# Kernel tuning notes

Hardware: AMD Instinct MI355X
Metric: run time of the kernel (lower is better)

The kernel has to match this reference:

```python
import jax, jax.numpy as jnp
import numpy as np

B, S, D, H = 4, 2048, 1024, 16
HD = D // H          # head_dim = 64
R = D // 2           # svd rank = int(D * svd_r), svd_r = 0.5


def setup_inputs() -> dict:
    key = jax.random.key(0)
    ks = jax.random.split(key, 12)
    sc = 0.02  # gpt2-style init scale
    return {
        "hidden_states": jax.random.normal(ks[0], (B, S, D), jnp.float32),
        # full Q projection (nn.Linear: weight [out, in])
        "WQ_w": jax.random.normal(ks[1], (D, D), jnp.float32) * sc,
        "WQ_b": jnp.zeros((D,), jnp.float32),
        # low-rank K projection: WK_A (no bias) then WK_B (bias)
        "WK_A_w": jax.random.normal(ks[2], (R, D), jnp.float32) * sc,
        "WK_B_w": jax.random.normal(ks[3], (D, R), jnp.float32) * sc,
        "WK_B_b": jnp.zeros((D,), jnp.float32),
        # low-rank V projection
        "WV_A_w": jax.random.normal(ks[4], (R, D), jnp.float32) * sc,
        "WV_B_w": jax.random.normal(ks[5], (D, R), jnp.float32) * sc,
        "WV_B_b": jnp.zeros((D,), jnp.float32),
        # output projection (HF Conv1D: weight [in, out], out = x @ W + b)
        "c_proj_w": jax.random.normal(ks[6], (D, D), jnp.float32) * sc,
        "c_proj_b": jnp.zeros((D,), jnp.float32),
    }


def reference(hidden_states, WQ_w, WQ_b, WK_A_w, WK_B_w, WK_B_b,
              WV_A_w, WV_B_w, WV_B_b, c_proj_w, c_proj_b):
    # projections (Q full-rank; K/V via SVD low-rank factors)
    q = hidden_states @ WQ_w.T + WQ_b                                  # [B,S,D]
    k = (hidden_states @ WK_A_w.T) @ WK_B_w.T + WK_B_b                 # [B,S,D]
    v = (hidden_states @ WV_A_w.T) @ WV_B_w.T + WV_B_b                 # [B,S,D]

    def split_heads(x):  # [B,S,D] -> [B,H,S,HD]
        return x.reshape(B, S, H, HD).transpose(0, 2, 1, 3)

    q, k, v = split_heads(q), split_heads(k), split_heads(v)

    # eager causal attention: QK^T / sqrt(head_dim), mask, softmax, PV
    scores = jnp.einsum('bhqd,bhkd->bhqk', q, k) / jnp.asarray(
        np.sqrt(HD), dtype=q.dtype)                                    # [B,H,S,S]
    causal = jnp.tril(jnp.ones((S, S), dtype=bool))
    scores = jnp.where(causal, scores, jnp.finfo(scores.dtype).min)
    attn = jax.nn.softmax(scores, axis=-1)                             # [B,H,S,S]
    # attn_dropout is identity (p=0 / eval mode)

    out = jnp.einsum('bhqk,bhkd->bqhd', attn, v).reshape(B, S, D)      # merge heads
    out = out @ c_proj_w + c_proj_b                                    # Conv1D c_proj
    # resid_dropout is identity (p=0 / eval mode)
    return out
```

## Files before the change

### kernel.cpp

```cpp
#include <hip/hip_runtime.h>

#define Bz 4
#define Sz 2048
#define Dz 1024
#define Hz 16
#define HDz 64
#define Rz 512
#define Mz (Bz * Sz)

typedef unsigned short u16;
typedef __bf16 bf16x8 __attribute__((ext_vector_type(8)));
typedef __bf16 bf16x4 __attribute__((ext_vector_type(4)));
typedef float f32x4 __attribute__((ext_vector_type(4)));
typedef u16 u16x8 __attribute__((ext_vector_type(8)));
typedef u16 u16x4 __attribute__((ext_vector_type(4)));

__device__ __forceinline__ u16 f2bf(float f) {
  unsigned u = __builtin_bit_cast(unsigned, f);
  u += 0x7fffu + ((u >> 16) & 1u);
  return (u16)(u >> 16);
}

#define GLDS(g, l)                                                              \
  __builtin_amdgcn_global_load_lds(                                             \
      (const __attribute__((address_space(1))) void*)(g),                       \
      (__attribute__((address_space(3))) void*)(l), 16, 0, 0)

__global__ void convert_bf16(const float* __restrict__ in, u16* __restrict__ out, int n) {
  int i = (blockIdx.x * blockDim.x + threadIdx.x) * 8;
  if (i >= n) return;
  float4 a = *(const float4*)(in + i);
  float4 b = *(const float4*)(in + i + 4);
  u16x8 r;
  r[0] = f2bf(a.x); r[1] = f2bf(a.y); r[2] = f2bf(a.z); r[3] = f2bf(a.w);
  r[4] = f2bf(b.x); r[5] = f2bf(b.y); r[6] = f2bf(b.z); r[7] = f2bf(b.w);
  *(u16x8*)(out + i) = r;
}

__global__ void transpose_convert(const float* __restrict__ in, u16* __restrict__ out,
                                  int R, int C) {
  __shared__ float t[32][33];
  int bx = blockIdx.x * 32, by = blockIdx.y * 32;
  int x = threadIdx.x, y = threadIdx.y;
#pragma unroll
  for (int j = 0; j < 32; j += 8) t[y + j][x] = in[(size_t)(by + y + j) * C + bx + x];
  __syncthreads();
#pragma unroll
  for (int j = 0; j < 32; j += 8)
    out[(size_t)(bx + y + j) * R + by + x] = f2bf(t[x][y + j]);
}

__global__ void make_biascat(const float* __restrict__ qb_, float* __restrict__ out) {
  int i = blockIdx.x * 256 + threadIdx.x;
  out[i] = (i < Dz) ? qb_[i] : 0.0f;
}

template <int MODE>
__global__ __launch_bounds__(256) void gemm_nt(const u16* __restrict__ A,
                                               const u16* __restrict__ W,
                                               const float* __restrict__ bias,
                                               void* __restrict__ Cv,
                                               int M, int N, int K, int lda) {
  __shared__ u16 As[128 * 32];
  __shared__ u16 Bs[128 * 32];
  const int tid = threadIdx.x;
  const int wid = tid >> 6, lane = tid & 63;
  const int nwg = gridDim.x * gridDim.y;
  const int id = blockIdx.y * gridDim.x + blockIdx.x;
  const int swz = (id & 7) * (nwg >> 3) + (id >> 3);
  const int bx = swz % gridDim.x, by = swz / gridDim.x;
  const int row0 = by * 128, col0 = bx * 128;
  const int wm = (wid >> 1) * 64, wn = (wid & 1) * 64;
  f32x4 acc[4][4] = {};
  const int srow = lane >> 2, scol = (lane & 3) * 8;
  const int frow = lane & 15, fk = (lane >> 4) * 8;

  for (int k0 = 0; k0 < K; k0 += 32) {
    __syncthreads();
#pragma unroll
    for (int it = 0; it < 2; ++it) {
      int c = it * 4 + wid;
      const u16* ga = A + (size_t)(row0 + c * 16 + srow) * lda + k0 + scol;
      const u16* gb = W + (size_t)(col0 + c * 16 + srow) * K + k0 + scol;
      GLDS(ga, As + c * 512);
      GLDS(gb, Bs + c * 512);
    }
    __syncthreads();
    bf16x8 af[4], bfr[4];
#pragma unroll
    for (int m = 0; m < 4; ++m) af[m] = *(const bf16x8*)(As + (wm + m * 16 + frow) * 32 + fk);
#pragma unroll
    for (int n = 0; n < 4; ++n) bfr[n] = *(const bf16x8*)(Bs + (wn + n * 16 + frow) * 32 + fk);
#pragma unroll
    for (int m = 0; m < 4; ++m)
#pragma unroll
      for (int n = 0; n < 4; ++n)
        acc[m][n] = __builtin_amdgcn_mfma_f32_16x16x32_bf16(af[m], bfr[n], acc[m][n], 0, 0, 0);
  }

  const int r4 = (lane >> 4) * 4, cc = lane & 15;
#pragma unroll
  for (int m = 0; m < 4; ++m)
#pragma unroll
    for (int n = 0; n < 4; ++n) {
      int col = col0 + wn + n * 16 + cc;
      float bv = bias[col];
      if constexpr (MODE == 2) {
        int rowb = row0 + wm + m * 16 + r4;
        size_t obase = (size_t)((rowb >> 11) * Hz + (col >> 6)) * ((size_t)HDz * Sz) +
                       (size_t)(col & 63) * Sz + (rowb & 2047);
        u16x4 w4;
#pragma unroll
        for (int j = 0; j < 4; ++j) w4[j] = f2bf(acc[m][n][j] + bv);
        *(u16x4*)((u16*)Cv + obase) = w4;
      } else {
#pragma unroll
        for (int j = 0; j < 4; ++j) {
          int row = row0 + wm + m * 16 + r4 + j;
          float v = acc[m][n][j] + bv;
          if constexpr (MODE == 0)
            ((u16*)Cv)[(size_t)row * N + col] = f2bf(v);
          else
            ((float*)Cv)[(size_t)row * N + col] = v;
        }
      }
    }
}

__device__ __forceinline__ void* lsw(void* base, int row, int bo) {
  return (char*)base + (((row << 7) + bo) ^ ((row & 7) << 4));
}

template <bool MASK>
__device__ __forceinline__ void tile_step(u16* Ks, u16* Vts, u16* Pw,
                                          int frow, int fhi, int qlocb, int koff,
                                          const bf16x8 (&qf)[2][2],
                                          f32x4 (&o)[4][2], float* rs) {
#pragma unroll
  for (int qs = 0; qs < 2; ++qs) {
    f32x4 s[4] = {};
#pragma unroll
    for (int dc = 0; dc < 2; ++dc)
#pragma unroll
      for (int c = 0; c < 4; ++c) {
        bf16x8 kf = *(const bf16x8*)lsw(Ks, c * 16 + frow, dc * 64 + fhi * 16);
        s[c] = __builtin_amdgcn_mfma_f32_16x16x32_bf16(kf, qf[qs][dc], s[c], 0, 0, 0);
      }
    const int qloc = qlocb + qs * 16 + frow;
#pragma unroll
    for (int c = 0; c < 4; ++c) {
      bf16x4 w;
#pragma unroll
      for (int j = 0; j < 4; ++j) {
        float v = __builtin_exp2f(s[c][j] * 0.18033688f);
        if (MASK) v = ((koff + c * 16 + fhi * 4 + j) <= qloc) ? v : 0.0f;
        rs[qs] += v;
        w[j] = (__bf16)v;
      }
      *(bf16x4*)lsw(Pw, qs * 16 + frow, c * 32 + fhi * 8) = w;
    }
  }
#pragma unroll
  for (int kc = 0; kc < 2; ++kc) {
    bf16x8 pa0 = *(const bf16x8*)lsw(Pw, frow, kc * 64 + fhi * 16);
    bf16x8 pa1 = *(const bf16x8*)lsw(Pw, 16 + frow, kc * 64 + fhi * 16);
#pragma unroll
    for (int n = 0; n < 4; ++n) {
      bf16x8 vf = *(const bf16x8*)lsw(Vts, n * 16 + frow, kc * 64 + fhi * 16);
      o[n][0] = __builtin_amdgcn_mfma_f32_16x16x32_bf16(vf, pa0, o[n][0], 0, 0, 0);
      o[n][1] = __builtin_amdgcn_mfma_f32_16x16x32_bf16(vf, pa1, o[n][1], 0, 0, 0);
    }
  }
}

__global__ __launch_bounds__(256, 2) void attn_kernel(const u16* __restrict__ Q,
                                                      const u16* __restrict__ Kg,
                                                      const u16* __restrict__ Vt,
                                                      u16* __restrict__ Og) {
  __shared__ __align__(16) u16 Ks[64 * 64];
  __shared__ __align__(16) u16 Vts[64 * 64];
  __shared__ __align__(16) u16 Ps[4][32 * 64];
  const int pr = blockIdx.x;
  const int qA = pr, qB = 15 - pr;
  const int bh = blockIdx.y;
  const int tid = threadIdx.x, wid = tid >> 6, lane = tid & 63;
  const size_t kbase = (size_t)(bh >> 4) * Sz * Dz + (size_t)(bh & 15) * HDz;
  const size_t qbase = (size_t)(bh >> 4) * Sz * 2048 + (size_t)(bh & 15) * HDz;
  const size_t vtb = (size_t)bh * HDz * Sz;
  const int frow = lane & 15, fhi = lane >> 4;
  const int q0A = qA * 128 + wid * 32, q0B = qB * 128 + wid * 32;

  bf16x8 qfA[2][2], qfB[2][2];
#pragma unroll
  for (int qs = 0; qs < 2; ++qs)
#pragma unroll
    for (int dc = 0; dc < 2; ++dc) {
      qfA[qs][dc] = *(const bf16x8*)(Q + qbase + (size_t)(q0A + qs * 16 + frow) * 2048 +
                                     dc * 32 + fhi * 8);
      qfB[qs][dc] = *(const bf16x8*)(Q + qbase + (size_t)(q0B + qs * 16 + frow) * 2048 +
                                     dc * 32 + fhi * 8);
    }

  f32x4 oA[4][2] = {}, oB[4][2] = {};
  float rsA[2] = {0.0f, 0.0f}, rsB[2] = {0.0f, 0.0f};

  const int r = tid >> 2, cb = (tid & 3) * 32;
  const u16* kgp = Kg + kbase + (size_t)r * Dz + (tid & 3) * 16;
  const u16* vgp = Vt + vtb + (size_t)r * Sz + (tid & 3) * 16;

  const int ntB = 2 * qB + 2;
  u16x8 ka = *(const u16x8*)(kgp);
  u16x8 kb2 = *(const u16x8*)(kgp + 8);
  u16x8 va = *(const u16x8*)(vgp);
  u16x8 vb2 = *(const u16x8*)(vgp + 8);

  for (int t = 0; t < ntB; ++t) {
    __syncthreads();
    *(u16x8*)lsw(Ks, r, cb) = ka;
    *(u16x8*)lsw(Ks, r, cb + 16) = kb2;
    *(u16x8*)lsw(Vts, r, cb) = va;
    *(u16x8*)lsw(Vts, r, cb + 16) = vb2;
    if (t + 1 < ntB) {
      const size_t ko = (size_t)(t + 1) * 64 * Dz;
      const size_t vo = (size_t)(t + 1) * 64;
      ka = *(const u16x8*)(kgp + ko);
      kb2 = *(const u16x8*)(kgp + ko + 8);
      va = *(const u16x8*)(vgp + vo);
      vb2 = *(const u16x8*)(vgp + vo + 8);
    }
    __syncthreads();

    if (64 * t <= q0B + 31) {
      if (t >= 2 * qB)
        tile_step<true>(Ks, Vts, Ps[wid], frow, fhi, wid * 32, (t - 2 * qB) * 64,
                        qfB, oB, rsB);
      else
        tile_step<false>(Ks, Vts, Ps[wid], frow, fhi, wid * 32, 0, qfB, oB, rsB);
    }
    if (64 * t <= q0A + 31) {
      if (t >= 2 * qA)
        tile_step<true>(Ks, Vts, Ps[wid], frow, fhi, wid * 32, (t - 2 * qA) * 64,
                        qfA, oA, rsA);
      else
        tile_step<false>(Ks, Vts, Ps[wid], frow, fhi, wid * 32, 0, qfA, oA, rsA);
    }
  }

#pragma unroll
  for (int x = 0; x < 2; ++x) {
    f32x4(&o)[4][2] = x ? oA : oB;
    float* rs = x ? rsA : rsB;
    const int q0 = x ? q0A : q0B;
#pragma unroll
    for (int qs = 0; qs < 2; ++qs) {
      float l = rs[qs];
      l += __shfl_xor(l, 16);
      l += __shfl_xor(l, 32);
      float inv = 1.0f / l;
      const size_t ob = kbase + (size_t)(q0 + qs * 16 + frow) * Dz;
#pragma unroll
      for (int n = 0; n < 4; ++n) {
        bf16x4 w;
#pragma unroll
        for (int j = 0; j < 4; ++j) w[j] = (__bf16)(o[n][qs][j] * inv);
        *(bf16x4*)(Og + ob + n * 16 + fhi * 4) = w;
      }
    }
  }
}

extern "C" void kernel_launch(void* const* d_in, const int* in_sizes, int n_in,
                              void* d_out, int out_size, void* d_ws, size_t ws_size,
                              hipStream_t stream) {
  const float* hs    = (const float*)d_in[0];
  const float* WQ_w  = (const float*)d_in[1];
  const float* WQ_b  = (const float*)d_in[2];
  const float* WKA_w = (const float*)d_in[3];
  const float* WKB_w = (const float*)d_in[4];
  const float* WKB_b = (const float*)d_in[5];
  const float* WVA_w = (const float*)d_in[6];
  const float* WVB_w = (const float*)d_in[7];
  const float* WVB_b = (const float*)d_in[8];
  const float* WC_w  = (const float*)d_in[9];
  const float* WC_b  = (const float*)d_in[10];
  float* out = (float*)d_out;

  char* p = (char*)d_ws;
  auto alloc = [&](size_t bytes) {
    char* r = p;
    p += (bytes + 255) & ~(size_t)255;
    return r;
  };
  u16* hsb   = (u16*)alloc((size_t)Mz * Dz * 2);
  u16* wcat  = (u16*)alloc((size_t)2048 * Dz * 2);
  u16* wkbb  = (u16*)alloc((size_t)Dz * Rz * 2);
  u16* wvbb  = (u16*)alloc((size_t)Dz * Rz * 2);
  u16* wcb   = (u16*)alloc((size_t)Dz * Dz * 2);
  float* bcat = (float*)alloc((size_t)2048 * 4);
  u16* QA    = (u16*)alloc((size_t)Mz * 2048 * 2);
  u16* Kb    = (u16*)alloc((size_t)Mz * Dz * 2);
  u16* Vtg   = (u16*)alloc((size_t)Mz * Dz * 2);
  u16* AOb   = hsb;

  convert_bf16<<<(Mz * Dz) / 8 / 256, 256, 0, stream>>>(hs, hsb, Mz * Dz);
  convert_bf16<<<(Dz * Dz) / 8 / 256, 256, 0, stream>>>(WQ_w, wcat, Dz * Dz);
  convert_bf16<<<(Rz * Dz) / 8 / 256, 256, 0, stream>>>(WKA_w, wcat + (size_t)Dz * Dz, Rz * Dz);
  convert_bf16<<<(Rz * Dz) / 8 / 256, 256, 0, stream>>>(WVA_w, wcat + (size_t)1536 * Dz, Rz * Dz);
  convert_bf16<<<(Dz * Rz) / 8 / 256, 256, 0, stream>>>(WKB_w, wkbb, Dz * Rz);
  convert_bf16<<<(Dz * Rz) / 8 / 256, 256, 0, stream>>>(WVB_w, wvbb, Dz * Rz);
  transpose_convert<<<dim3(Dz / 32, Dz / 32), dim3(32, 8), 0, stream>>>(WC_w, wcb, Dz, Dz);
  make_biascat<<<8, 256, 0, stream>>>(WQ_b, bcat);

  gemm_nt<0><<<dim3(2048 / 128, Mz / 128), 256, 0, stream>>>(hsb, wcat, bcat, QA,
                                                             Mz, 2048, Dz, Dz);
  gemm_nt<0><<<dim3(Dz / 128, Mz / 128), 256, 0, stream>>>(QA + Dz, wkbb, WKB_b, Kb,
                                                           Mz, Dz, Rz, 2048);
  gemm_nt<2><<<dim3(Dz / 128, Mz / 128), 256, 0, stream>>>(QA + 1536, wvbb, WVB_b, Vtg,
                                                           Mz, Dz, Rz, 2048);

  attn_kernel<<<dim3(Sz / 256, Bz * Hz), 256, 0, stream>>>(QA, Kb, Vtg, AOb);

  gemm_nt<1><<<dim3(Dz / 128, Mz / 128), 256, 0, stream>>>(AOb, wcb, WC_b, out,
                                                           Mz, Dz, Dz, Dz);
}
```

Measured before the change: 311.3 us.

## Add 256x256 tiled GEMM kernel and batch K/V up-projections into one launch

Adds a new GEMM kernel with 256x256 output tiles, 512 threads, 64-wide K steps, double-buffered LDS fed by global_load_lds, an XOR-swizzled LDS layout, workgroup id swizzling and raised MFMA priority. The QKV-A projection now uses it, and the K and V up-projections run together in one launch, selected by blockIdx.z. The old gemm_nt keeps only the fp32 output mode for c_proj. The aim is more data reuse per tile and fewer launches. The cost is much more LDS per block and more registers per thread, which could reduce occupancy.

Result: faster. 282.0 us (-9.4%).

```diff
diff --git a/kernel.cpp b/kernel.cpp
--- a/kernel.cpp
+++ b/kernel.cpp
@@ -105,8 +105,107 @@
     for (int n = 0; n < 4; ++n) {
       int col = col0 + wn + n * 16 + cc;
       float bv = bias[col];
-      if constexpr (MODE == 2) {
-        int rowb = row0 + wm + m * 16 + r4;
+#pragma unroll
+      for (int j = 0; j < 4; ++j) {
+        int row = row0 + wm + m * 16 + r4 + j;
+        ((float*)Cv)[(size_t)row * N + col] = acc[m][n][j] + bv;
+      }
+    }
+}
+
+__global__ __launch_bounds__(512, 2) void gemm256(
+    const u16* __restrict__ A0, const u16* __restrict__ W0,
+    const float* __restrict__ bias0, void* __restrict__ C0, int mode0,
+    const u16* __restrict__ A1, const u16* __restrict__ W1,
+    const float* __restrict__ bias1, void* __restrict__ C1, int mode1,
+    int N, int K, int lda) {
+  __shared__ __align__(16) u16 As[2][256 * 64];
+  __shared__ __align__(16) u16 Bs[2][256 * 64];
+  const int z = blockIdx.z;
+  const u16* A = z ? A1 : A0;
+  const u16* W = z ? W1 : W0;
+  const float* bias = z ? bias1 : bias0;
+  void* Cv = z ? C1 : C0;
+  const int mode = z ? mode1 : mode0;
+
+  const int tid = threadIdx.x, wid = tid >> 6, lane = tid & 63;
+  const int gx = gridDim.x;
+  const int nwg = gx * gridDim.y;
+  const int id = blockIdx.y * gx + blockIdx.x;
+  const int swz = (id & 7) * (nwg >> 3) + (id >> 3);
+  const int bx = swz % gx, by = swz / gx;
+  const int row0 = by * 256, col0 = bx * 256;
+  const int wr = wid >> 2, wc = wid & 3;
+  const int frow = lane & 15, fhi = lane >> 4;
+
+  const u16* ap[4];
+  const u16* bp[4];
+#pragma unroll
+  for (int rnd = 0; rnd < 4; ++rnd) {
+    int P = rnd * 8192 + tid * 16;
+    int L = P ^ (((P >> 7) & 7) << 4);
+    int r = L >> 7, c = (L & 127) >> 1;
+    ap[rnd] = A + (size_t)(row0 + r) * lda + c;
+    bp[rnd] = W + (size_t)(col0 + r) * K + c;
+  }
+
+  auto stage = [&](int buf, int kt) {
+    const int k0 = kt * 64;
+#pragma unroll
+    for (int rnd = 0; rnd < 4; ++rnd) {
+      GLDS(ap[rnd] + k0, &As[buf][rnd * 4096 + tid * 8]);
+      GLDS(bp[rnd] + k0, &Bs[buf][rnd * 4096 + tid * 8]);
+    }
+  };
+  auto rd = [](const u16* base, int row, int colb) -> bf16x8 {
+    int off = ((row << 7) + colb) ^ ((row & 7) << 4);
+    return *(const bf16x8*)((const char*)base + off);
+  };
+
+  f32x4 acc[8][4] = {};
+  const int NT = K >> 6;
+  stage(0, 0);
+  __syncthreads();
+  int cur = 0;
+  for (int kt = 0; kt < NT; ++kt) {
+    if (kt + 1 < NT) stage(cur ^ 1, kt + 1);
+    bf16x8 bfr[2][4];
+#pragma unroll
+    for (int ks = 0; ks < 2; ++ks)
+#pragma unroll
+      for (int n = 0; n < 4; ++n)
+        bfr[ks][n] = rd(Bs[cur], wc * 64 + n * 16 + frow, ks * 64 + fhi * 16);
+    __builtin_amdgcn_s_setprio(1);
+#pragma unroll
+    for (int mg = 0; mg < 4; ++mg) {
+      bf16x8 af[2][2];
+#pragma unroll
+      for (int mi = 0; mi < 2; ++mi)
+#pragma unroll
+        for (int ks = 0; ks < 2; ++ks)
+          af[mi][ks] = rd(As[cur], wr * 128 + mg * 32 + mi * 16 + frow, ks * 64 + fhi * 16);
+#pragma unroll
+      for (int mi = 0; mi < 2; ++mi)
+#pragma unroll
+        for (int ks = 0; ks < 2; ++ks)
+#pragma unroll
+          for (int n = 0; n < 4; ++n)
+            acc[mg * 2 + mi][n] = __builtin_amdgcn_mfma_f32_16x16x32_bf16(
+                af[mi][ks], bfr[ks][n], acc[mg * 2 + mi][n], 0, 0, 0);
+    }
+    __builtin_amdgcn_s_setprio(0);
+    __syncthreads();
+    cur ^= 1;
+  }
+
+#pragma unroll
+  for (int m = 0; m < 8; ++m)
+#pragma unroll
+    for (int n = 0; n < 4; ++n) {
+      const int col = col0 + wc * 64 + n * 16 + frow;
+      const int rowb = row0 + wr * 128 + m * 16 + fhi * 4;
+      const float bv = bias[col];
+      if (mode == 2) {
         size_t obase = (size_t)((rowb >> 11) * Hz + (col >> 6)) * ((size_t)HDz * Sz) +
                        (size_t)(col & 63) * Sz + (rowb & 2047);
         u16x4 w4;
@@ -115,14 +214,8 @@
         *(u16x4*)((u16*)Cv + obase) = w4;
       } else {
 #pragma unroll
-        for (int j = 0; j < 4; ++j) {
-          int row = row0 + wm + m * 16 + r4 + j;
-          float v = acc[m][n][j] + bv;
-          if constexpr (MODE == 0)
-            ((u16*)Cv)[(size_t)row * N + col] = f2bf(v);
-          else
-            ((float*)Cv)[(size_t)row * N + col] = v;
-        }
+        for (int j = 0; j < 4; ++j)
+          ((u16*)Cv)[(size_t)(rowb + j) * N + col] = f2bf(acc[m][n][j] + bv);
       }
     }
 }
@@ -311,12 +404,12 @@
   transpose_convert<<<dim3(Dz / 32, Dz / 32), dim3(32, 8), 0, stream>>>(WC_w, wcb, Dz, Dz);
   make_biascat<<<8, 256, 0, stream>>>(WQ_b, bcat);
 
-  gemm_nt<0><<<dim3(2048 / 128, Mz / 128), 256, 0, stream>>>(hsb, wcat, bcat, QA,
-                                                             Mz, 2048, Dz, Dz);
-  gemm_nt<0><<<dim3(Dz / 128, Mz / 128), 256, 0, stream>>>(QA + Dz, wkbb, WKB_b, Kb,
-                                                           Mz, Dz, Rz, 2048);
-  gemm_nt<2><<<dim3(Dz / 128, Mz / 128), 256, 0, stream>>>(QA + 1536, wvbb, WVB_b, Vtg,
-                                                           Mz, Dz, Rz, 2048);
+  gemm256<<<dim3(2048 / 256, Mz / 256, 1), 512, 0, stream>>>(
+      hsb, wcat, bcat, QA, 0, hsb, wcat, bcat, QA, 0, 2048, Dz, Dz);
+
+  gemm256<<<dim3(Dz / 256, Mz / 256, 2), 512, 0, stream>>>(
+      QA + Dz, wkbb, WKB_b, Kb, 0,
+      QA + 1536, wvbb, WVB_b, Vtg, 2, Dz, Rz, 2048);
 
   attn_kernel<<<dim3(Sz / 256, Bz * Hz), 256, 0, stream>>>(QA, Kb, Vtg, AOb);
 
```

## Replace GEMMs with 256-wide multi-stage pipelined kernel and fold softmax scale into Q

Applied to the files above, without the earlier changes.

Replaces the single-buffered 128x128 GEMM with a 512-thread kernel using 256-column tiles, a 4-slot LDS ring with global_load_lds prefetch three steps ahead, XOR-swizzled shared layout and explicit waitcnt/barrier scheduling. The K and V up-projections are merged into one launch via blockIdx.z, and the output projection uses a 128-row variant. The softmax scale is folded into the Q weights and bias during conversion, removing a multiply in the attention inner loop. These aim to cut global-load latency stalls, bank conflicts and launch count, at the cost of more LDS per block and lower occupancy, plus extra rounding from scaling Q before the bf16 cast.

New measurement: 279.2 us. 1.12x faster.

```diff
diff --git a/kernel.cpp b/kernel.cpp
--- a/kernel.cpp
+++ b/kernel.cpp
@@ -26,14 +26,17 @@
       (const __attribute__((address_space(1))) void*)(g),                       \
       (__attribute__((address_space(3))) void*)(l), 16, 0, 0)
 
-__global__ void convert_bf16(const float* __restrict__ in, u16* __restrict__ out, int n) {
+__global__ void convert_bf16(const float* __restrict__ in, u16* __restrict__ out,
+                             int n, float scale) {
   int i = (blockIdx.x * blockDim.x + threadIdx.x) * 8;
   if (i >= n) return;
   float4 a = *(const float4*)(in + i);
   float4 b = *(const float4*)(in + i + 4);
   u16x8 r;
-  r[0] = f2bf(a.x); r[1] = f2bf(a.y); r[2] = f2bf(a.z); r[3] = f2bf(a.w);
-  r[4] = f2bf(b.x); r[5] = f2bf(b.y); r[6] = f2bf(b.z); r[7] = f2bf(b.w);
+  r[0] = f2bf(a.x * scale); r[1] = f2bf(a.y * scale);
+  r[2] = f2bf(a.z * scale); r[3] = f2bf(a.w * scale);
+  r[4] = f2bf(b.x * scale); r[5] = f2bf(b.y * scale);
+  r[6] = f2bf(b.z * scale); r[7] = f2bf(b.w * scale);
   *(u16x8*)(out + i) = r;
 }
 
@@ -52,77 +55,129 @@
 
 __global__ void make_biascat(const float* __restrict__ qb_, float* __restrict__ out) {
   int i = blockIdx.x * 256 + threadIdx.x;
-  out[i] = (i < Dz) ? qb_[i] : 0.0f;
-}
-
-template <int MODE>
-__global__ __launch_bounds__(256) void gemm_nt(const u16* __restrict__ A,
-                                               const u16* __restrict__ W,
-                                               const float* __restrict__ bias,
-                                               void* __restrict__ Cv,
-                                               int M, int N, int K, int lda) {
-  __shared__ u16 As[128 * 32];
-  __shared__ u16 Bs[128 * 32];
-  const int tid = threadIdx.x;
-  const int wid = tid >> 6, lane = tid & 63;
-  const int nwg = gridDim.x * gridDim.y;
-  const int id = blockIdx.y * gridDim.x + blockIdx.x;
+  out[i] = (i < Dz) ? qb_[i] * 0.18033688f : 0.0f;
+}
+
+template <int BM>
+__global__ __launch_bounds__(512, 2) void gemm256(
+    const u16* __restrict__ A0, const u16* __restrict__ W0,
+    const float* __restrict__ bias0, void* __restrict__ C0, int mode0,
+    const u16* __restrict__ A1, const u16* __restrict__ W1,
+    const float* __restrict__ bias1, void* __restrict__ C1, int mode1,
+    int N, int K, int lda) {
+  constexpr int MF = BM / 32;
+  constexpr int ARND = BM / 128;
+  __shared__ __align__(16) u16 As[4][BM * 32];
+  __shared__ __align__(16) u16 Bs[4][256 * 32];
+
+  const int z = blockIdx.z;
+  const u16* A = z ? A1 : A0;
+  const u16* W = z ? W1 : W0;
+  const float* bias = z ? bias1 : bias0;
+  void* Cv = z ? C1 : C0;
+  const int mode = z ? mode1 : mode0;
+
+  const int tid = threadIdx.x, wid = tid >> 6, lane = tid & 63;
+  const int gx = gridDim.x;
+  const int nwg = gx * gridDim.y;
+  const int id = blockIdx.y * gx + blockIdx.x;
   const int swz = (id & 7) * (nwg >> 3) + (id >> 3);
-  const int bx = swz % gridDim.x, by = swz / gridDim.x;
-  const int row0 = by * 128, col0 = bx * 128;
-  const int wm = (wid >> 1) * 64, wn = (wid & 1) * 64;
-  f32x4 acc[4][4] = {};
-  const int srow = lane >> 2, scol = (lane & 3) * 8;
-  const int frow = lane & 15, fk = (lane >> 4) * 8;
-
-  for (int k0 = 0; k0 < K; k0 += 32) {
-    __syncthreads();
-#pragma unroll
-    for (int it = 0; it < 2; ++it) {
-      int c = it * 4 + wid;
-      const u16* ga = A + (size_t)(row0 + c * 16 + srow) * lda + k0 + scol;
-      const u16* gb = W + (size_t)(col0 + c * 16 + srow) * K + k0 + scol;
-      GLDS(ga, As + c * 512);
-      GLDS(gb, Bs + c * 512);
-    }
-    __syncthreads();
-    bf16x8 af[4], bfr[4];
-#pragma unroll
-    for (int m = 0; m < 4; ++m) af[m] = *(const bf16x8*)(As + (wm + m * 16 + frow) * 32 + fk);
-#pragma unroll
-    for (int n = 0; n < 4; ++n) bfr[n] = *(const bf16x8*)(Bs + (wn + n * 16 + frow) * 32 + fk);
-#pragma unroll
-    for (int m = 0; m < 4; ++m)
+  const int bx = swz % gx, by = swz / gx;
+  const int row0 = by * BM, col0 = bx * 256;
+  const int wr = wid >> 2, wc = wid & 3;
+  const int frow = lane & 15, fhi = lane >> 4;
+
+  const u16* ap[ARND];
+  const u16* bp[2];
+#pragma unroll
+  for (int rnd = 0; rnd < 2; ++rnd) {
+    int P = rnd * 8192 + tid * 16;
+    int l6 = ((P >> 6) ^ (P >> 8)) & 1;
+    int l5 = ((P >> 5) ^ (P >> 7)) & 1;
+    int l4 = ((P >> 4) & 1) ^ l6;
+    int L = (P & ~0x70) | (l6 << 6) | (l5 << 5) | (l4 << 4);
+    int row = L >> 6, colu = (L & 63) >> 1;
+    if (rnd < ARND) ap[rnd] = A + (size_t)(row0 + row) * lda + colu;
+    bp[rnd] = W + (size_t)(col0 + row) * K + colu;
+  }
+
+  const int H = K >> 5;
+  auto stage = [&](int h) {
+    const int off = h * 32;
+    const int slot = h & 3;
+#pragma unroll
+    for (int rnd = 0; rnd < ARND; ++rnd)
+      GLDS(ap[rnd] + off, &As[slot][rnd * 4096 + tid * 8]);
+#pragma unroll
+    for (int rnd = 0; rnd < 2; ++rnd)
+      GLDS(bp[rnd] + off, &Bs[slot][rnd * 4096 + tid * 8]);
+  };
+  auto rd = [](const u16* base, int row, int bo) -> bf16x8 {
+    int L = (row << 6) + bo;
+    int P = L ^ ((L >> 2) & 0x70);
+    return *(const bf16x8*)((const char*)base + P);
+  };
+
+  f32x4 acc[MF][4] = {};
+
+  stage(0); stage(1); stage(2);
+
+  auto body = [&](int h, bool mainphase) {
+    asm volatile("s_waitcnt lgkmcnt(0)" ::: "memory");
+    if (mainphase) {
+      if constexpr (BM == 256)
+        asm volatile("s_waitcnt vmcnt(8)" ::: "memory");
+      else
+        asm volatile("s_waitcnt vmcnt(6)" ::: "memory");
+    } else {
+      asm volatile("s_waitcnt vmcnt(0)" ::: "memory");
+    }
+    __builtin_amdgcn_s_barrier();
+    __builtin_amdgcn_sched_barrier(0);
+    const int slot = h & 3;
+    bf16x8 bfr[4];
+#pragma unroll
+    for (int n = 0; n < 4; ++n)
+      bfr[n] = rd(Bs[slot], wc * 64 + n * 16 + frow, fhi * 16);
+    bf16x8 af[MF];
+#pragma unroll
+    for (int m = 0; m < MF; ++m)
+      af[m] = rd(As[slot], wr * (BM / 2) + m * 16 + frow, fhi * 16);
+    if (mainphase) stage(h + 3);
+    __builtin_amdgcn_s_setprio(1);
+#pragma unroll
+    for (int m = 0; m < MF; ++m)
 #pragma unroll
       for (int n = 0; n < 4; ++n)
         acc[m][n] = __builtin_amdgcn_mfma_f32_16x16x32_bf16(af[m], bfr[n], acc[m][n], 0, 0, 0);
-  }
-
-  const int r4 = (lane >> 4) * 4, cc = lane & 15;
-#pragma unroll
-  for (int m = 0; m < 4; ++m)
+    __builtin_amdgcn_s_setprio(0);
+  };
+
+  for (int h = 0; h < H - 3; ++h) body(h, true);
+  for (int h = H - 3; h < H; ++h) body(h, false);
+
+#pragma unroll
+  for (int m = 0; m < MF; ++m)
 #pragma unroll
     for (int n = 0; n < 4; ++n) {
-      int col = col0 + wn + n * 16 + cc;
-      float bv = bias[col];
-      if constexpr (MODE == 2) {
-        int rowb = row0 + wm + m * 16 + r4;
+      const int col = col0 + wc * 64 + n * 16 + frow;
+      const int rowb = row0 + wr * (BM / 2) + m * 16 + fhi * 4;
+      const float bv = bias[col];
+      if (mode == 2) {
         size_t obase = (size_t)((rowb >> 11) * Hz + (col >> 6)) * ((size_t)HDz * Sz) +
                        (size_t)(col & 63) * Sz + (rowb & 2047);
         u16x4 w4;
 #pragma unroll
         for (int j = 0; j < 4; ++j) w4[j] = f2bf(acc[m][n][j] + bv);
         *(u16x4*)((u16*)Cv + obase) = w4;
+      } else if (mode == 1) {
+#pragma unroll
+        for (int j = 0; j < 4; ++j)
+          ((float*)Cv)[(size_t)(rowb + j) * N + col] = acc[m][n][j] + bv;
       } else {
 #pragma unroll
-        for (int j = 0; j < 4; ++j) {
-          int row = row0 + wm + m * 16 + r4 + j;
-          float v = acc[m][n][j] + bv;
-          if constexpr (MODE == 0)
-            ((u16*)Cv)[(size_t)row * N + col] = f2bf(v);
-          else
-            ((float*)Cv)[(size_t)row * N + col] = v;
-        }
+        for (int j = 0; j < 4; ++j)
+          ((u16*)Cv)[(size_t)(rowb + j) * N + col] = f2bf(acc[m][n][j] + bv);
       }
     }
 }
@@ -152,7 +207,7 @@
       bf16x4 w;
 #pragma unroll
       for (int j = 0; j < 4; ++j) {
-        float v = __builtin_exp2f(s[c][j] * 0.18033688f);
+        float v = __builtin_exp2f(s[c][j]);
         if (MASK) v = ((koff + c * 16 + fhi * 4 + j) <= qloc) ? v : 0.0f;
         rs[qs] += v;
         w[j] = (__bf16)v;
@@ -302,24 +357,28 @@
   u16* Vtg   = (u16*)alloc((size_t)Mz * Dz * 2);
   u16* AOb   = hsb;
 
-  convert_bf16<<<(Mz * Dz) / 8 / 256, 256, 0, stream>>>(hs, hsb, Mz * Dz);
-  convert_bf16<<<(Dz * Dz) / 8 / 256, 256, 0, stream>>>(WQ_w, wcat, Dz * Dz);
-  convert_bf16<<<(Rz * Dz) / 8 / 256, 256, 0, stream>>>(WKA_w, wcat + (size_t)Dz * Dz, Rz * Dz);
-  convert_bf16<<<(Rz * Dz) / 8 / 256, 256, 0, stream>>>(WVA_w, wcat + (size_t)1536 * Dz, Rz * Dz);
-  convert_bf16<<<(Dz * Rz) / 8 / 256, 256, 0, stream>>>(WKB_w, wkbb, Dz * Rz);
-  convert_bf16<<<(Dz * Rz) / 8 / 256, 256, 0, stream>>>(WVB_w, wvbb, Dz * Rz);
+  const float SC = 0.18033688f;
+
+  convert_bf16<<<(Mz * Dz) / 8 / 256, 256, 0, stream>>>(hs, hsb, Mz * Dz, 1.0f);
+  convert_bf16<<<(Dz * Dz) / 8 / 256, 256, 0, stream>>>(WQ_w, wcat, Dz * Dz, SC);
+  convert_bf16<<<(Rz * Dz) / 8 / 256, 256, 0, stream>>>(WKA_w, wcat + (size_t)Dz * Dz,
+                                                        Rz * Dz, 1.0f);
+  convert_bf16<<<(Rz * Dz) / 8 / 256, 256, 0, stream>>>(WVA_w, wcat + (size_t)1536 * Dz,
+                                                        Rz * Dz, 1.0f);
+  convert_bf16<<<(Dz * Rz) / 8 / 256, 256, 0, stream>>>(WKB_w, wkbb, Dz * Rz, 1.0f);
+  convert_bf16<<<(Dz * Rz) / 8 / 256, 256, 0, stream>>>(WVB_w, wvbb, Dz * Rz, 1.0f);
   transpose_convert<<<dim3(Dz / 32, Dz / 32), dim3(32, 8), 0, stream>>>(WC_w, wcb, Dz, Dz);
   make_biascat<<<8, 256, 0, stream>>>(WQ_b, bcat);
 
-  gemm_nt<0><<<dim3(2048 / 128, Mz / 128), 256, 0, stream>>>(hsb, wcat, bcat, QA,
-                                                             Mz, 2048, Dz, Dz);
-  gemm_nt<0><<<dim3(Dz / 128, Mz / 128), 256, 0, stream>>>(QA + Dz, wkbb, WKB_b, Kb,
-                                                           Mz, Dz, Rz, 2048);
-  gemm_nt<2><<<dim3(Dz / 128, Mz / 128), 256, 0, stream>>>(QA + 1536, wvbb, WVB_b, Vtg,
-                                                           Mz, Dz, Rz, 2048);
+  gemm256<256><<<dim3(2048 / 256, Mz / 256, 1), 512, 0, stream>>>(
+      hsb, wcat, bcat, QA, 0, hsb, wcat, bcat, QA, 0, 2048, Dz, Dz);
+
+  gemm256<256><<<dim3(Dz / 256, Mz / 256, 2), 512, 0, stream>>>(
+      QA + Dz, wkbb, WKB_b, Kb, 0,
+      QA + 1536, wvbb, WVB_b, Vtg, 2, Dz, Rz, 2048);
 
   attn_kernel<<<dim3(Sz / 256, Bz * Hz), 256, 0, stream>>>(QA, Kb, Vtg, AOb);
 
-  gemm_nt<1><<<dim3(Dz / 128, Mz / 128), 256, 0, stream>>>(AOb, wcb, WC_b, out,
-                                                           Mz, Dz, Dz, Dz);
-}
+  gemm256<128><<<dim3(Dz / 256, Mz / 128, 1), 512, 0, stream>>>(
+      AOb, wcb, WC_b, out, 1, AOb, wcb, WC_b, out, 1, Dz, Dz, Dz);
+}
```
